# Kernel optimization log

Hardware: AMD Instinct MI355X
Metric: run time of the kernel (lower is better)

## Reference

```python
import jax, jax.numpy as jnp
import numpy as np

NEG_INF = -1.0e9
VALID_THRESH = -1.0e8
EPS = 1e-12


def _l2_normalize(x):
    n = jnp.linalg.norm(x, axis=-1, keepdims=True)
    return x / jnp.maximum(n, EPS)


def setup_inputs() -> dict:
    key = jax.random.key(0)
    k1, k2, k3, k4 = jax.random.split(key, 4)
    B, Nq, Nd, D = 64, 32, 256, 128
    return {
        "query_embeds": jax.random.normal(k1, (B, Nq, D), dtype=jnp.float32),
        "query_mask": jax.random.randint(k2, (B, Nq), 0, 2, dtype=jnp.int32),
        "doc_embeds": jax.random.normal(k3, (B, Nd, D), dtype=jnp.float32),
        "doc_mask": jax.random.randint(k4, (B, Nd), 0, 2, dtype=jnp.int32),
    }


def reference(query_embeds, query_mask, doc_embeds, doc_mask):
    # normalize=True, symmetric=True path
    q = _l2_normalize(query_embeds)
    d = _l2_normalize(doc_embeds)
    qm = query_mask.astype(jnp.float32)[..., None]  # [B, Nq, 1]
    dm = doc_mask.astype(jnp.float32)[..., None]    # [B, Nd, 1]
    q = q * qm
    d = d * dm

    # token_sims: [Bq, Bd, Nq, Nd]
    token_sims = jnp.einsum("qtd,csd->qcts", q, d)
    # pair mask: [Bq,1,Nq,1] * [1,Bd,1,Nd]
    mask = qm[:, None, :, :] * dm[None, :, :, 0][:, :, None, :].transpose(1, 0, 2, 3)
    masked_sims = jnp.where(mask > 0, token_sims, NEG_INF)

    # query -> doc max over doc tokens
    q2d = jnp.max(masked_sims, axis=-1)          # [Bq, Bd, Nq]
    valid_q = (q2d > VALID_THRESH).astype(jnp.float32)
    q2d = jnp.where(valid_q > 0, q2d, 0.0)
    cnt_q = jnp.maximum(jnp.sum(valid_q, axis=-1), 1.0)
    q2d_score = jnp.sum(q2d, axis=-1) / cnt_q    # [Bq, Bd]

    # doc -> query max over query tokens
    d2q = jnp.max(masked_sims, axis=-2)          # [Bq, Bd, Nd]
    valid_d = (d2q > VALID_THRESH).astype(jnp.float32)
    d2q = jnp.where(valid_d > 0, d2q, 0.0)
    cnt_d = jnp.maximum(jnp.sum(valid_d, axis=-1), 1.0)
    d2q_score = jnp.sum(d2q, axis=-1) / cnt_d    # [Bq, Bd]

    return (q2d_score + d2q_score) / 2.0
```

## Files before the change

kernel.cpp:

```cpp
#include <hip/hip_runtime.h>
#include <hip/hip_bf16.h>
#include <stdint.h>

typedef short bf16x8 __attribute__((ext_vector_type(8)));
typedef short short8 __attribute__((ext_vector_type(8)));
typedef float f32x4 __attribute__((ext_vector_type(4)));

#define B_   64
#define NQ   32
#define ND   256
#define DIM  128
#define MT   4
#define NEG_INF_F (-1.0e9f)
#define VALID_F   (-1.0e8f)

__global__ __launch_bounds__(256) void qnorm(
    const float* __restrict__ q, const int* __restrict__ qmask,
    __hip_bfloat16* __restrict__ qn)
{
    const int tid = threadIdx.x;
    const int sub = tid & 15;
    const int row = blockIdx.x * 16 + (tid >> 4);

    const float* src = q + (size_t)row * DIM;
    const float4 v0 = *reinterpret_cast<const float4*>(src + sub * 8);
    const float4 v1 = *reinterpret_cast<const float4*>(src + sub * 8 + 4);
    float ss = v0.x*v0.x + v0.y*v0.y + v0.z*v0.z + v0.w*v0.w
             + v1.x*v1.x + v1.y*v1.y + v1.z*v1.z + v1.w*v1.w;
    #pragma unroll
    for (int off = 1; off <= 8; off <<= 1) ss += __shfl_xor(ss, off);

    const float scale = qmask[row] ? (1.0f / fmaxf(sqrtf(ss), 1e-12f)) : 0.0f;

    short8 o;
    const float f[8] = {v0.x, v0.y, v0.z, v0.w, v1.x, v1.y, v1.z, v1.w};
    #pragma unroll
    for (int j = 0; j < 8; ++j) {
        __hip_bfloat16 b = __float2bfloat16(f[j] * scale);
        o[j] = *reinterpret_cast<short*>(&b);
    }
    *reinterpret_cast<short8*>(qn + (size_t)row * DIM + sub * 8) = o;
}

__global__ __launch_bounds__(256) void chamfer_fused(
    const float* __restrict__ d,
    const __hip_bfloat16* __restrict__ qn,
    const int* __restrict__ qmask,
    const int* __restrict__ dmask,
    float* __restrict__ out)
{
    __shared__ __hip_bfloat16 ldsD[ND * DIM];
    __shared__ float s_cmax[MT][ND];
    __shared__ float s_rmaxT[MT][NQ][4];

    const int bd  = blockIdx.x & 63;
    const int g   = blockIdx.x >> 6;
    const int tid = threadIdx.x;
    const int w   = tid >> 6;
    const int l   = tid & 63;
    const int lr  = l & 15;
    const int lk  = l >> 4;

    {
        const float* Dsrc = d + (size_t)bd * ND * DIM;
        const int sub = tid & 15;
        const int rb  = tid >> 4;
        #pragma unroll
        for (int it = 0; it < 16; ++it) {
            const int row = it * 16 + rb;
            const float4 v0 = *reinterpret_cast<const float4*>(Dsrc + row * DIM + sub * 8);
            const float4 v1 = *reinterpret_cast<const float4*>(Dsrc + row * DIM + sub * 8 + 4);
            float ss = v0.x*v0.x + v0.y*v0.y + v0.z*v0.z + v0.w*v0.w
                     + v1.x*v1.x + v1.y*v1.y + v1.z*v1.z + v1.w*v1.w;
            #pragma unroll
            for (int off = 1; off <= 8; off <<= 1) ss += __shfl_xor(ss, off);
            const float scale = dmask[bd * ND + row] ? (1.0f / fmaxf(sqrtf(ss), 1e-12f)) : 0.0f;
            short8 o;
            const float f[8] = {v0.x, v0.y, v0.z, v0.w, v1.x, v1.y, v1.z, v1.w};
            #pragma unroll
            for (int j = 0; j < 8; ++j) {
                __hip_bfloat16 b = __float2bfloat16(f[j] * scale);
                o[j] = *reinterpret_cast<short*>(&b);
            }
            *reinterpret_cast<short8*>((char*)&ldsD[0] + row * 256 + ((sub ^ (row & 7)) << 4)) = o;
        }
    }
    __syncthreads();

    #pragma unroll 1
    for (int mm = 0; mm < 4; ++mm) {
        const int bq0 = g * 16 + mm * MT;

        int4 qm4[MT][2];
        int  dmv[MT][4];
        #pragma unroll
        for (int m = 0; m < MT; ++m) {
            #pragma unroll
            for (int mi = 0; mi < 2; ++mi)
                qm4[m][mi] = *reinterpret_cast<const int4*>(&qmask[(bq0 + m) * NQ + mi * 16 + lk * 4]);
            #pragma unroll
            for (int ni = 0; ni < 4; ++ni)
                dmv[m][ni] = dmask[(bq0 + m) * ND + w * 64 + ni * 16 + lr];
        }

        f32x4 acc[MT][2][4] = {};
        #pragma unroll
        for (int kk = 0; kk < 4; ++kk) {
            const int k0   = kk * 32 + lk * 8;
            const int cL   = kk * 4 + lk;
            bf16x8 bfr[4];
            #pragma unroll
            for (int ni = 0; ni < 4; ++ni) {
                const int rowd = w * 64 + ni * 16 + lr;
                bfr[ni] = *reinterpret_cast<const bf16x8*>(
                    (const char*)&ldsD[0] + rowd * 256 + ((cL ^ (rowd & 7)) << 4));
            }
            #pragma unroll
            for (int m = 0; m < MT; ++m) {
                const __hip_bfloat16* Q = qn + (size_t)(bq0 + m) * (NQ * DIM);
                #pragma unroll
                for (int mi = 0; mi < 2; ++mi) {
                    const bf16x8 a = *reinterpret_cast<const bf16x8*>(Q + (mi * 16 + lr) * DIM + k0);
                    #pragma unroll
                    for (int ni = 0; ni < 4; ++ni)
                        acc[m][mi][ni] = __builtin_amdgcn_mfma_f32_16x16x32_bf16(a, bfr[ni], acc[m][mi][ni], 0, 0, 0);
                }
            }
        }

        #pragma unroll
        for (int m = 0; m < MT; ++m) {
            float rmax[2][4];
            float cmax[4];
            #pragma unroll
            for (int ni = 0; ni < 4; ++ni) cmax[ni] = NEG_INF_F;
            #pragma unroll
            for (int mi = 0; mi < 2; ++mi) {
                const int qmr[4] = {qm4[m][mi].x, qm4[m][mi].y, qm4[m][mi].z, qm4[m][mi].w};
                #pragma unroll
                for (int r = 0; r < 4; ++r) {
                    float rm = NEG_INF_F;
                    #pragma unroll
                    for (int ni = 0; ni < 4; ++ni) {
                        const float v = (qmr[r] && dmv[m][ni]) ? acc[m][mi][ni][r] : NEG_INF_F;
                        rm = fmaxf(rm, v);
                        cmax[ni] = fmaxf(cmax[ni], v);
                    }
                    rmax[mi][r] = rm;
                }
            }
            #pragma unroll
            for (int ni = 0; ni < 4; ++ni) {
                cmax[ni] = fmaxf(cmax[ni], __shfl_xor(cmax[ni], 16));
                cmax[ni] = fmaxf(cmax[ni], __shfl_xor(cmax[ni], 32));
            }
            if (lk == 0) {
                #pragma unroll
                for (int ni = 0; ni < 4; ++ni)
                    s_cmax[m][w * 64 + ni * 16 + lr] = cmax[ni];
            }
            #pragma unroll
            for (int mi = 0; mi < 2; ++mi)
                #pragma unroll
                for (int r = 0; r < 4; ++r) {
                    #pragma unroll
                    for (int off = 1; off <= 8; off <<= 1)
                        rmax[mi][r] = fmaxf(rmax[mi][r], __shfl_xor(rmax[mi][r], off));
                }
            if (lr == 0) {
                #pragma unroll
                for (int mi = 0; mi < 2; ++mi)
                    #pragma unroll
                    for (int r = 0; r < 4; ++r)
                        s_rmaxT[m][mi * 16 + lk * 4 + r][w] = rmax[mi][r];
            }
        }
        __syncthreads();

        {
            const int m = w;
            const float4 cm = *reinterpret_cast<const float4*>(&s_cmax[m][l * 4]);
            float sd = 0.0f, cd = 0.0f;
            if (cm.x > VALID_F) { sd += cm.x; cd += 1.0f; }
            if (cm.y > VALID_F) { sd += cm.y; cd += 1.0f; }
            if (cm.z > VALID_F) { sd += cm.z; cd += 1.0f; }
            if (cm.w > VALID_F) { sd += cm.w; cd += 1.0f; }
            float sq = 0.0f, cq = 0.0f;
            if (l < NQ) {
                const float4 rm4 = *reinterpret_cast<const float4*>(&s_rmaxT[m][l][0]);
                const float v = fmaxf(fmaxf(rm4.x, rm4.y), fmaxf(rm4.z, rm4.w));
                if (v > VALID_F) { sq = v; cq = 1.0f; }
            }
            #pragma unroll
            for (int off = 1; off <= 32; off <<= 1) {
                sd += __shfl_xor(sd, off);
                cd += __shfl_xor(cd, off);
                sq += __shfl_xor(sq, off);
                cq += __shfl_xor(cq, off);
            }
            if (l == 0) {
                const float q2d = sq / fmaxf(cq, 1.0f);
                const float d2q = sd / fmaxf(cd, 1.0f);
                out[(bq0 + m) * B_ + bd] = 0.5f * (q2d + d2q);
            }
        }
        __syncthreads();
    }
}

extern "C" void kernel_launch(void* const* d_in, const int* in_sizes, int n_in,
                              void* d_out, int out_size, void* d_ws, size_t ws_size,
                              hipStream_t stream) {
    const float* q  = (const float*)d_in[0];
    const int*   qm = (const int*)d_in[1];
    const float* d  = (const float*)d_in[2];
    const int*   dm = (const int*)d_in[3];
    float* out = (float*)d_out;

    __hip_bfloat16* qn = (__hip_bfloat16*)d_ws;

    qnorm<<<(B_ * NQ) / 16, 256, 0, stream>>>(q, qm, qn);
    chamfer_fused<<<B_ * 4, 256, 0, stream>>>(d, qn, qm, dm, out);
}
```

Measured before the change: 116.0 us.

## Fuse query normalization into chamfer kernel and stage Q in LDS with 8 waves

Removes the separate qnorm launch. Each block now normalizes its four query batches itself, writes them as bf16 into a swizzled LDS tile, and reads MFMA A-operands from LDS instead of global memory. The block grows to 512 threads so each wave covers 32 doc rows instead of 64, and one __syncthreads per loop iteration is dropped. In exchange, query normalization is recomputed redundantly by every doc block, and LDS use grows to roughly 104KB, which likely limits the kernel to one block per CU.

```diff
diff --git a/kernel.cpp b/kernel.cpp
--- a/kernel.cpp
+++ b/kernel.cpp
@@ -14,44 +14,17 @@
 #define NEG_INF_F (-1.0e9f)
 #define VALID_F   (-1.0e8f)
 
-__global__ __launch_bounds__(256) void qnorm(
-    const float* __restrict__ q, const int* __restrict__ qmask,
-    __hip_bfloat16* __restrict__ qn)
-{
-    const int tid = threadIdx.x;
-    const int sub = tid & 15;
-    const int row = blockIdx.x * 16 + (tid >> 4);
-
-    const float* src = q + (size_t)row * DIM;
-    const float4 v0 = *reinterpret_cast<const float4*>(src + sub * 8);
-    const float4 v1 = *reinterpret_cast<const float4*>(src + sub * 8 + 4);
-    float ss = v0.x*v0.x + v0.y*v0.y + v0.z*v0.z + v0.w*v0.w
-             + v1.x*v1.x + v1.y*v1.y + v1.z*v1.z + v1.w*v1.w;
-    #pragma unroll
-    for (int off = 1; off <= 8; off <<= 1) ss += __shfl_xor(ss, off);
-
-    const float scale = qmask[row] ? (1.0f / fmaxf(sqrtf(ss), 1e-12f)) : 0.0f;
-
-    short8 o;
-    const float f[8] = {v0.x, v0.y, v0.z, v0.w, v1.x, v1.y, v1.z, v1.w};
-    #pragma unroll
-    for (int j = 0; j < 8; ++j) {
-        __hip_bfloat16 b = __float2bfloat16(f[j] * scale);
-        o[j] = *reinterpret_cast<short*>(&b);
-    }
-    *reinterpret_cast<short8*>(qn + (size_t)row * DIM + sub * 8) = o;
-}
-
-__global__ __launch_bounds__(256) void chamfer_fused(
+__global__ __launch_bounds__(512, 2) void chamfer_one(
+    const float* __restrict__ q,
+    const int* __restrict__ qmask,
     const float* __restrict__ d,
-    const __hip_bfloat16* __restrict__ qn,
-    const int* __restrict__ qmask,
     const int* __restrict__ dmask,
     float* __restrict__ out)
 {
     __shared__ __hip_bfloat16 ldsD[ND * DIM];
+    __shared__ __hip_bfloat16 ldsQ[4 * NQ * DIM];
     __shared__ float s_cmax[MT][ND];
-    __shared__ float s_rmaxT[MT][NQ][4];
+    __shared__ float s_rmaxT[MT][NQ][8];
 
     const int bd  = blockIdx.x & 63;
     const int g   = blockIdx.x >> 6;
@@ -60,14 +33,14 @@
     const int l   = tid & 63;
     const int lr  = l & 15;
     const int lk  = l >> 4;
+    const int grp = tid >> 4;
+    const int sub = tid & 15;
 
     {
         const float* Dsrc = d + (size_t)bd * ND * DIM;
-        const int sub = tid & 15;
-        const int rb  = tid >> 4;
-        #pragma unroll
-        for (int it = 0; it < 16; ++it) {
-            const int row = it * 16 + rb;
+        #pragma unroll
+        for (int it = 0; it < 8; ++it) {
+            const int row = it * 32 + grp;
             const float4 v0 = *reinterpret_cast<const float4*>(Dsrc + row * DIM + sub * 8);
             const float4 v1 = *reinterpret_cast<const float4*>(Dsrc + row * DIM + sub * 8 + 4);
             float ss = v0.x*v0.x + v0.y*v0.y + v0.z*v0.z + v0.w*v0.w
@@ -82,47 +55,71 @@
                 __hip_bfloat16 b = __float2bfloat16(f[j] * scale);
                 o[j] = *reinterpret_cast<short*>(&b);
             }
-            *reinterpret_cast<short8*>((char*)&ldsD[0] + row * 256 + ((sub ^ (row & 7)) << 4)) = o;
+            *reinterpret_cast<short8*>((char*)&ldsD[0] + row * 256 + (((sub ^ (row & 7)) & 15) << 4)) = o;
         }
     }
-    __syncthreads();
 
     #pragma unroll 1
     for (int mm = 0; mm < 4; ++mm) {
         const int bq0 = g * 16 + mm * MT;
 
+        {
+            const float* Qsrc = q + (size_t)bq0 * NQ * DIM;
+            #pragma unroll
+            for (int it = 0; it < 4; ++it) {
+                const int row = it * 32 + grp;
+                const float4 v0 = *reinterpret_cast<const float4*>(Qsrc + row * DIM + sub * 8);
+                const float4 v1 = *reinterpret_cast<const float4*>(Qsrc + row * DIM + sub * 8 + 4);
+                float ss = v0.x*v0.x + v0.y*v0.y + v0.z*v0.z + v0.w*v0.w
+                         + v1.x*v1.x + v1.y*v1.y + v1.z*v1.z + v1.w*v1.w;
+                #pragma unroll
+                for (int off = 1; off <= 8; off <<= 1) ss += __shfl_xor(ss, off);
+                const float scale = qmask[bq0 * NQ + row] ? (1.0f / fmaxf(sqrtf(ss), 1e-12f)) : 0.0f;
+                short8 o;
+                const float f[8] = {v0.x, v0.y, v0.z, v0.w, v1.x, v1.y, v1.z, v1.w};
+                #pragma unroll
+                for (int j = 0; j < 8; ++j) {
+                    __hip_bfloat16 b = __float2bfloat16(f[j] * scale);
+                    o[j] = *reinterpret_cast<short*>(&b);
+                }
+                *reinterpret_cast<short8*>((char*)&ldsQ[0] + row * 256 + (((sub ^ (row & 7)) & 15) << 4)) = o;
+            }
+        }
+
         int4 qm4[MT][2];
-        int  dmv[MT][4];
+        int  dmv[MT][2];
         #pragma unroll
         for (int m = 0; m < MT; ++m) {
             #pragma unroll
             for (int mi = 0; mi < 2; ++mi)
                 qm4[m][mi] = *reinterpret_cast<const int4*>(&qmask[(bq0 + m) * NQ + mi * 16 + lk * 4]);
             #pragma unroll
-            for (int ni = 0; ni < 4; ++ni)
-                dmv[m][ni] = dmask[(bq0 + m) * ND + w * 64 + ni * 16 + lr];
-        }
-
-        f32x4 acc[MT][2][4] = {};
+            for (int ni = 0; ni < 2; ++ni)
+                dmv[m][ni] = dmask[(bq0 + m) * ND + w * 32 + ni * 16 + lr];
+        }
+
+        __syncthreads();
+
+        f32x4 acc[MT][2][2] = {};
         #pragma unroll
         for (int kk = 0; kk < 4; ++kk) {
-            const int k0   = kk * 32 + lk * 8;
-            const int cL   = kk * 4 + lk;
-            bf16x8 bfr[4];
-            #pragma unroll
-            for (int ni = 0; ni < 4; ++ni) {
-                const int rowd = w * 64 + ni * 16 + lr;
+            const int cL = kk * 4 + lk;
+            bf16x8 bfr[2];
+            #pragma unroll
+            for (int ni = 0; ni < 2; ++ni) {
+                const int rowd = w * 32 + ni * 16 + lr;
                 bfr[ni] = *reinterpret_cast<const bf16x8*>(
-                    (const char*)&ldsD[0] + rowd * 256 + ((cL ^ (rowd & 7)) << 4));
+                    (const char*)&ldsD[0] + rowd * 256 + (((cL ^ (rowd & 7)) & 15) << 4));
             }
             #pragma unroll
             for (int m = 0; m < MT; ++m) {
-                const __hip_bfloat16* Q = qn + (size_t)(bq0 + m) * (NQ * DIM);
                 #pragma unroll
                 for (int mi = 0; mi < 2; ++mi) {
-                    const bf16x8 a = *reinterpret_cast<const bf16x8*>(Q + (mi * 16 + lr) * DIM + k0);
-                    #pragma unroll
-                    for (int ni = 0; ni < 4; ++ni)
+                    const int rowq = m * NQ + mi * 16 + lr;
+                    const bf16x8 a = *reinterpret_cast<const bf16x8*>(
+                        (const char*)&ldsQ[0] + rowq * 256 + (((cL ^ (rowq & 7)) & 15) << 4));
+                    #pragma unroll
+                    for (int ni = 0; ni < 2; ++ni)
                         acc[m][mi][ni] = __builtin_amdgcn_mfma_f32_16x16x32_bf16(a, bfr[ni], acc[m][mi][ni], 0, 0, 0);
                 }
             }
@@ -131,9 +128,9 @@
         #pragma unroll
         for (int m = 0; m < MT; ++m) {
             float rmax[2][4];
-            float cmax[4];
-            #pragma unroll
-            for (int ni = 0; ni < 4; ++ni) cmax[ni] = NEG_INF_F;
+            float cmax[2];
+            #pragma unroll
+            for (int ni = 0; ni < 2; ++ni) cmax[ni] = NEG_INF_F;
             #pragma unroll
             for (int mi = 0; mi < 2; ++mi) {
                 const int qmr[4] = {qm4[m][mi].x, qm4[m][mi].y, qm4[m][mi].z, qm4[m][mi].w};
@@ -141,7 +138,7 @@
                 for (int r = 0; r < 4; ++r) {
                     float rm = NEG_INF_F;
                     #pragma unroll
-                    for (int ni = 0; ni < 4; ++ni) {
+                    for (int ni = 0; ni < 2; ++ni) {
                         const float v = (qmr[r] && dmv[m][ni]) ? acc[m][mi][ni][r] : NEG_INF_F;
                         rm = fmaxf(rm, v);
                         cmax[ni] = fmaxf(cmax[ni], v);
@@ -150,14 +147,14 @@
                 }
             }
             #pragma unroll
-            for (int ni = 0; ni < 4; ++ni) {
+            for (int ni = 0; ni < 2; ++ni) {
                 cmax[ni] = fmaxf(cmax[ni], __shfl_xor(cmax[ni], 16));
                 cmax[ni] = fmaxf(cmax[ni], __shfl_xor(cmax[ni], 32));
             }
             if (lk == 0) {
                 #pragma unroll
-                for (int ni = 0; ni < 4; ++ni)
-                    s_cmax[m][w * 64 + ni * 16 + lr] = cmax[ni];
+                for (int ni = 0; ni < 2; ++ni)
+                    s_cmax[m][w * 32 + ni * 16 + lr] = cmax[ni];
             }
             #pragma unroll
             for (int mi = 0; mi < 2; ++mi)
@@ -177,7 +174,7 @@
         }
         __syncthreads();
 
-        {
+        if (w < MT) {
             const int m = w;
             const float4 cm = *reinterpret_cast<const float4*>(&s_cmax[m][l * 4]);
             float sd = 0.0f, cd = 0.0f;
@@ -187,8 +184,10 @@
             if (cm.w > VALID_F) { sd += cm.w; cd += 1.0f; }
             float sq = 0.0f, cq = 0.0f;
             if (l < NQ) {
-                const float4 rm4 = *reinterpret_cast<const float4*>(&s_rmaxT[m][l][0]);
-                const float v = fmaxf(fmaxf(rm4.x, rm4.y), fmaxf(rm4.z, rm4.w));
+                const float4 a = *reinterpret_cast<const float4*>(&s_rmaxT[m][l][0]);
+                const float4 b = *reinterpret_cast<const float4*>(&s_rmaxT[m][l][4]);
+                const float v = fmaxf(fmaxf(fmaxf(a.x, a.y), fmaxf(a.z, a.w)),
+                                      fmaxf(fmaxf(b.x, b.y), fmaxf(b.z, b.w)));
                 if (v > VALID_F) { sq = v; cq = 1.0f; }
             }
             #pragma unroll
@@ -204,7 +203,6 @@
                 out[(bq0 + m) * B_ + bd] = 0.5f * (q2d + d2q);
             }
         }
-        __syncthreads();
     }
 }
 
@@ -217,8 +215,5 @@
     const int*   dm = (const int*)d_in[3];
     float* out = (float*)d_out;
 
-    __hip_bfloat16* qn = (__hip_bfloat16*)d_ws;
-
-    qnorm<<<(B_ * NQ) / 16, 256, 0, stream>>>(q, qm, qn);
-    chamfer_fused<<<B_ * 4, 256, 0, stream>>>(d, qn, qm, dm, out);
+    chamfer_one<<<B_ * 4, 512, 0, stream>>>(q, qm, d, dm, out);
 }
```

Result: faster. 102.4 us (-11.8%).
